# Kernel tuning notes

Hardware: AMD Instinct MI355X
Metric: run time of the kernel (lower is better)

## Reference

```python
import jax, jax.numpy as jnp
import numpy as np

NS, B, D_MODEL = 512, 2, 512
NH, DH = 8, 64
LEAKY_SLOPE = 0.01  # torch nn.LeakyReLU default


def setup_inputs() -> dict:
    key = jax.random.key(0)
    ks = jax.random.split(key, 6)
    scale = 1.0 / np.sqrt(D_MODEL)
    query = jax.random.normal(ks[0], (NS, B, D_MODEL), dtype=jnp.float32)
    W_q = jax.random.normal(ks[1], (D_MODEL, NH * DH), dtype=jnp.float32) * scale
    b_q = jnp.zeros((NH * DH,), dtype=jnp.float32)
    W_k = jax.random.normal(ks[2], (D_MODEL, NH * DH), dtype=jnp.float32) * scale
    b_k = jnp.zeros((NH * DH,), dtype=jnp.float32)
    # xavier_uniform over [NH, DH]
    bound = np.sqrt(6.0 / (NH + DH))
    scoring_proj = jax.random.uniform(ks[3], (NH, DH), minval=-bound, maxval=bound, dtype=jnp.float32)
    return {"query": query, "W_q": W_q, "b_q": b_q, "W_k": W_k, "b_k": b_k,
            "scoring_proj": scoring_proj}


def reference(query, W_q, b_q, W_k, b_k, scoring_proj):
    # query: [ns, b, d_model]
    q = query @ W_q + b_q  # [ns, b, nh*dh]
    k = query @ W_k + b_k  # [ns, b, nh*dh]
    # 'ns b (nh dh) -> b ns nh dh'
    q = jnp.transpose(q.reshape(NS, B, NH, DH), (1, 0, 2, 3))  # [b, ns, nh, dh]
    k = jnp.transpose(k.reshape(NS, B, NH, DH), (1, 0, 2, 3))  # [b, ns, nh, dh]
    # broadcast add: [b, q, k, nh, dh]
    s = q[:, :, None, :, :] + k[:, None, :, :, :]
    s = jnp.where(s >= 0, s, LEAKY_SLOPE * s)  # LeakyReLU
    attn = jnp.einsum('bqkhe,he->bhqk', s, scoring_proj)
    # k rearranged '(b nh) ns dh'
    k_out = jnp.transpose(k, (0, 2, 1, 3)).reshape(B * NH, NS, DH)
    return attn, k_out
```

## Files before the change

kernel.cpp:

```cpp
#include <hip/hip_runtime.h>

#define NS 512
#define DM 512
#define NH 8
#define DH 64
#define NHDH 512
#define ATTN_SIZE (2 * NH * NS * NS)

typedef __attribute__((ext_vector_type(8))) _Float16 half8;
typedef __attribute__((ext_vector_type(4))) float f32x4;
typedef _Float16 h2 __attribute__((ext_vector_type(2)));
typedef unsigned short ushort_t;
typedef __attribute__((ext_vector_type(2))) unsigned uint2v;

#if defined(__has_builtin)
#if __has_builtin(__builtin_amdgcn_fdot2)
#define HAVE_FDOT2 1
#endif
#if __has_builtin(__builtin_amdgcn_cvt_pkrtz)
#define HAVE_PKRTZ 1
#endif
#endif

__device__ __forceinline__ unsigned pkh(float a, float b) {
#ifdef HAVE_PKRTZ
    auto r = __builtin_amdgcn_cvt_pkrtz(a, b);
    return __builtin_bit_cast(unsigned, r);
#else
    h2 r; r[0] = (_Float16)a; r[1] = (_Float16)b;
    return __builtin_bit_cast(unsigned, r);
#endif
}

__device__ __forceinline__ float qdot2(unsigned w2, unsigned x2, float acc) {
#ifdef HAVE_FDOT2
    return __builtin_amdgcn_fdot2(__builtin_bit_cast(h2, w2),
                                  __builtin_bit_cast(h2, x2), acc, false);
#else
    h2 a = __builtin_bit_cast(h2, w2);
    h2 b = __builtin_bit_cast(h2, x2);
    return acc + (float)a[0] * (float)b[0] + (float)a[1] * (float)b[1];
#endif
}

__device__ __forceinline__ float dotabs(unsigned w2, unsigned q2, unsigned k2, float acc) {
    h2 s = __builtin_bit_cast(h2, q2) + __builtin_bit_cast(h2, k2);
    unsigned a = __builtin_bit_cast(unsigned, s) & 0x7FFF7FFFu;
    return qdot2(w2, a, acc);
}

__global__ __launch_bounds__(256) void proj_fused(
    const float* __restrict__ query,
    const float* __restrict__ Wq, const float* __restrict__ bq,
    const float* __restrict__ Wk, const float* __restrict__ bk,
    ushort_t* __restrict__ qh, ushort_t* __restrict__ kh,
    float* __restrict__ kout)
{
    const int h  = blockIdx.x;
    const int by = blockIdx.y;
    const int bz = blockIdx.z;
    const float* __restrict__ W   = bz ? Wk : Wq;
    const float* __restrict__ bia = bz ? bk : bq;
    ushort_t* __restrict__ hout = bz ? kh : qh;

    __shared__ __align__(16) ushort_t As[64][136];
    __shared__ __align__(16) ushort_t Bs[64][136];

    const int tid  = threadIdx.x;
    const int lane = tid & 63;
    const int wv   = __builtin_amdgcn_readfirstlane(tid >> 6);
    const int wr   = wv >> 1, wc = wv & 1;
    const int l15  = lane & 15, l4 = lane >> 4;

    float4 af[4][2];
    float  bf[8][4];
    #pragma unroll
    for (int i = 0; i < 4; ++i) {
        int s = i * 256 + tid;
        const float* src = query + (size_t)(by * 64 + (s >> 4)) * DM + (s & 15) * 8;
        af[i][0] = *(const float4*)(src);
        af[i][1] = *(const float4*)(src + 4);
    }
    #pragma unroll
    for (int p = 0; p < 8; ++p)
        #pragma unroll
        for (int j = 0; j < 4; ++j)
            bf[p][j] = W[(size_t)(p * 16 + (tid >> 6) * 4 + j) * NHDH + h * 64 + lane];

    f32x4 acc[2][2];
    #pragma unroll
    for (int f = 0; f < 2; ++f)
        #pragma unroll
        for (int g = 0; g < 2; ++g) acc[f][g] = (f32x4){0.f, 0.f, 0.f, 0.f};

    for (int kc = 0; kc < 4; ++kc) {
        __syncthreads();
        #pragma unroll
        for (int i = 0; i < 4; ++i) {
            int s = i * 256 + tid;
            uint4 pk;
            pk.x = pkh(af[i][0].x, af[i][0].y);
            pk.y = pkh(af[i][0].z, af[i][0].w);
            pk.z = pkh(af[i][1].x, af[i][1].y);
            pk.w = pkh(af[i][1].z, af[i][1].w);
            *(uint4*)&As[s >> 4][(s & 15) * 8] = pk;
        }
        #pragma unroll
        for (int p = 0; p < 8; ++p) {
            uint2v pk;
            pk.x = pkh(bf[p][0], bf[p][1]);
            pk.y = pkh(bf[p][2], bf[p][3]);
            *(uint2v*)&Bs[lane][p * 16 + (tid >> 6) * 4] = pk;
        }
        __syncthreads();
        if (kc < 3) {
            #pragma unroll
            for (int i = 0; i < 4; ++i) {
                int s = i * 256 + tid;
                const float* src = query + (size_t)(by * 64 + (s >> 4)) * DM
                                 + (kc + 1) * 128 + (s & 15) * 8;
                af[i][0] = *(const float4*)(src);
                af[i][1] = *(const float4*)(src + 4);
            }
            #pragma unroll
            for (int p = 0; p < 8; ++p)
                #pragma unroll
                for (int j = 0; j < 4; ++j)
                    bf[p][j] = W[(size_t)((kc + 1) * 128 + p * 16 + (tid >> 6) * 4 + j) * NHDH
                                 + h * 64 + lane];
        }
        #pragma unroll
        for (int ks = 0; ks < 4; ++ks) {
            half8 a0 = *(const half8*)&As[wr * 32 + l15     ][ks * 32 + l4 * 8];
            half8 a1 = *(const half8*)&As[wr * 32 + 16 + l15][ks * 32 + l4 * 8];
            half8 b0 = *(const half8*)&Bs[wc * 32 + l15     ][ks * 32 + l4 * 8];
            half8 b1 = *(const half8*)&Bs[wc * 32 + 16 + l15][ks * 32 + l4 * 8];
            acc[0][0] = __builtin_amdgcn_mfma_f32_16x16x32_f16(a0, b0, acc[0][0], 0, 0, 0);
            acc[0][1] = __builtin_amdgcn_mfma_f32_16x16x32_f16(a0, b1, acc[0][1], 0, 0, 0);
            acc[1][0] = __builtin_amdgcn_mfma_f32_16x16x32_f16(a1, b0, acc[1][0], 0, 0, 0);
            acc[1][1] = __builtin_amdgcn_mfma_f32_16x16x32_f16(a1, b1, acc[1][1], 0, 0, 0);
        }
    }

    const float bias0 = bia[h * 64 + wc * 32 + l15];
    const float bias1 = bia[h * 64 + wc * 32 + 16 + l15];
    #pragma unroll
    for (int f = 0; f < 2; ++f)
        #pragma unroll
        for (int g = 0; g < 2; ++g) {
            float bg = g ? bias1 : bias0;
            #pragma unroll
            for (int j = 0; j < 4; ++j) {
                int rt = wr * 32 + f * 16 + l4 * 4 + j;
                int ct = wc * 32 + g * 16 + l15;
                int rg = by * 64 + rt;
                int ns_ = rg >> 1, b_ = rg & 1;
                size_t idx = ((size_t)(b_ * NH + h) * NS + ns_) * DH + ct;
                float vv = acc[f][g][j] + bg;
                if (bz) kout[idx] = vv;
                _Float16 hv = (_Float16)vv;
                hout[idx] = __builtin_bit_cast(ushort_t, hv);
            }
        }
}

__global__ __launch_bounds__(256, 4) void attn3_kernel(
    const ushort_t* __restrict__ qh,
    const ushort_t* __restrict__ kh,
    const float* __restrict__ w,
    float* __restrict__ attn)
{
    __shared__ __align__(16) ushort_t Qs[32][72];

    const int tid  = threadIdx.x;
    const int lane = tid & 63;
    const int wv   = tid >> 6;
    const int bid  = blockIdx.x;
    const int kb   = bid & 3;
    const int bh   = (bid >> 2) & 15;
    const int qt   = bid >> 6;
    const int h    = bh & 7;

    const int c0 = kb * 128 + lane;
    const ushort_t* kb0 = kh + (size_t)bh * NS * DH + (size_t)c0 * DH;
    __align__(16) unsigned kr0[32], kr1[32];
    #pragma unroll
    for (int i = 0; i < 8; ++i)
        *(uint4*)&kr0[i * 4] = *(const uint4*)(kb0 + i * 8);
    #pragma unroll
    for (int i = 0; i < 8; ++i)
        *(uint4*)&kr1[i * 4] = *(const uint4*)(kb0 + 64 * DH + i * 8);

    {
        const uint4* qsrc = (const uint4*)(qh + (size_t)bh * NS * DH + (size_t)qt * 32 * DH);
        int row = tid >> 3, col = (tid & 7) * 8;
        *(uint4*)&Qs[row][col] = qsrc[tid];
    }

    unsigned wp[32];
    const float* wrow = w + h * DH;
    #pragma unroll
    for (int i = 0; i < 16; ++i) {
        float4 v = *(const float4*)(wrow + i * 4);
        _Float16 a = (_Float16)v.x, b = (_Float16)v.y, c = (_Float16)v.z, d = (_Float16)v.w;
        unsigned lo = (unsigned)__builtin_bit_cast(ushort_t, a) |
                      ((unsigned)__builtin_bit_cast(ushort_t, b) << 16);
        unsigned hi = (unsigned)__builtin_bit_cast(ushort_t, c) |
                      ((unsigned)__builtin_bit_cast(ushort_t, d) << 16);
        wp[2 * i]     = __builtin_amdgcn_readfirstlane(lo);
        wp[2 * i + 1] = __builtin_amdgcn_readfirstlane(hi);
    }

    float kd0 = 0.f, kd1 = 0.f;
    #pragma unroll
    for (int p = 0; p < 32; ++p) {
        kd0 = qdot2(wp[p], kr0[p], kd0);
        kd1 = qdot2(wp[p], kr1[p], kd1);
    }

    __syncthreads();

    float* obase = attn + (size_t)bh * NS * NS
                 + (size_t)(qt * 32 + wv * 8) * NS + kb * 128 + lane;

    #pragma unroll 2
    for (int r = 0; r < 8; ++r) {
        const int row = wv * 8 + r;
        __align__(16) unsigned q2a[32];
        #pragma unroll
        for (int i = 0; i < 8; ++i)
            *(uint4*)&q2a[i * 4] = *((const uint4*)&Qs[row][0] + i);

        float qd0 = 0.f, qd1 = 0.f;
        #pragma unroll
        for (int p = 0; p < 16; ++p) {
            qd0 = qdot2(wp[2 * p],     q2a[2 * p],     qd0);
            qd1 = qdot2(wp[2 * p + 1], q2a[2 * p + 1], qd1);
        }
        const float qd = qd0 + qd1;

        float a0 = 0.f, a1 = 0.f;
        #pragma unroll
        for (int p = 0; p < 32; ++p) {
            const unsigned q2 = q2a[p], w2 = wp[p];
            a0 = dotabs(w2, q2, kr0[p], a0);
            a1 = dotabs(w2, q2, kr1[p], a1);
        }

        float* ob = obase + r * NS;
        ob[0]  = fmaf(0.495f, a0, 0.505f * (qd + kd0));
        ob[64] = fmaf(0.495f, a1, 0.505f * (qd + kd1));
    }
}

extern "C" void kernel_launch(void* const* d_in, const int* in_sizes, int n_in,
                              void* d_out, int out_size, void* d_ws, size_t ws_size,
                              hipStream_t stream) {
    const float* query = (const float*)d_in[0];
    const float* Wq    = (const float*)d_in[1];
    const float* bq    = (const float*)d_in[2];
    const float* Wk    = (const float*)d_in[3];
    const float* bk    = (const float*)d_in[4];
    const float* w     = (const float*)d_in[5];

    float* attn = (float*)d_out;
    float* kout = (float*)d_out + ATTN_SIZE;

    char* ws = (char*)d_ws;
    ushort_t* qh = (ushort_t*)(ws);
    ushort_t* kh = (ushort_t*)(ws + (1u << 20));

    proj_fused<<<dim3(NH, 16, 2), 256, 0, stream>>>(query, Wq, bq, Wk, bk, qh, kh, kout);
    attn3_kernel<<<1024, 256, 0, stream>>>(qh, kh, w, attn);
}
```

Measured before the change: 33.61 us.

## Fuse projection and attention into one cooperative kernel with grid sync

Merges the projection and attention kernels into a single cooperative launch of 512 blocks that uses a grid-wide barrier between the two phases. Work is rebalanced so both phases use 512 blocks: projection tiles drop to 32 rows and attention blocks cover 64 query rows each. This is meant to remove the second kernel launch and the gap between kernels. In exchange it adds a grid barrier, per-call host queries for device attributes and occupancy, and lower per-block parallelism, with a two-kernel fallback if the cooperative launch is unavailable.

```diff
diff --git a/kernel.cpp b/kernel.cpp
--- a/kernel.cpp
+++ b/kernel.cpp
@@ -1,4 +1,7 @@
 #include <hip/hip_runtime.h>
+#include <hip/hip_cooperative_groups.h>
+
+namespace cg = cooperative_groups;
 
 #define NS 512
 #define DM 512
@@ -6,6 +9,7 @@
 #define DH 64
 #define NHDH 512
 #define ATTN_SIZE (2 * NH * NS * NS)
+#define SMEM_BYTES 26112
 
 typedef __attribute__((ext_vector_type(8))) _Float16 half8;
 typedef __attribute__((ext_vector_type(4))) float f32x4;
@@ -49,35 +53,34 @@
     return qdot2(w2, a, acc);
 }
 
-__global__ __launch_bounds__(256) void proj_fused(
+__device__ __forceinline__ void phase_proj(int bid, int tid,
     const float* __restrict__ query,
     const float* __restrict__ Wq, const float* __restrict__ bq,
     const float* __restrict__ Wk, const float* __restrict__ bk,
     ushort_t* __restrict__ qh, ushort_t* __restrict__ kh,
-    float* __restrict__ kout)
-{
-    const int h  = blockIdx.x;
-    const int by = blockIdx.y;
-    const int bz = blockIdx.z;
+    float* __restrict__ kout, char* smem)
+{
+    const int h   = bid & 7;
+    const int byt = (bid >> 3) & 31;
+    const int bz  = bid >> 8;
     const float* __restrict__ W   = bz ? Wk : Wq;
     const float* __restrict__ bia = bz ? bk : bq;
     ushort_t* __restrict__ hout = bz ? kh : qh;
 
-    __shared__ __align__(16) ushort_t As[64][136];
-    __shared__ __align__(16) ushort_t Bs[64][136];
-
-    const int tid  = threadIdx.x;
+    ushort_t (*As)[136] = (ushort_t(*)[136])smem;
+    ushort_t (*Bs)[136] = (ushort_t(*)[136])(smem + 32 * 136 * 2);
+
     const int lane = tid & 63;
-    const int wv   = __builtin_amdgcn_readfirstlane(tid >> 6);
-    const int wr   = wv >> 1, wc = wv & 1;
+    const int w4   = tid >> 6;
+    const int wr   = w4 >> 1, wc = w4 & 1;
     const int l15  = lane & 15, l4 = lane >> 4;
 
-    float4 af[4][2];
+    float4 af[2][2];
     float  bf[8][4];
     #pragma unroll
-    for (int i = 0; i < 4; ++i) {
+    for (int i = 0; i < 2; ++i) {
         int s = i * 256 + tid;
-        const float* src = query + (size_t)(by * 64 + (s >> 4)) * DM + (s & 15) * 8;
+        const float* src = query + (size_t)(byt * 32 + (s >> 4)) * DM + (s & 15) * 8;
         af[i][0] = *(const float4*)(src);
         af[i][1] = *(const float4*)(src + 4);
     }
@@ -85,18 +88,16 @@
     for (int p = 0; p < 8; ++p)
         #pragma unroll
         for (int j = 0; j < 4; ++j)
-            bf[p][j] = W[(size_t)(p * 16 + (tid >> 6) * 4 + j) * NHDH + h * 64 + lane];
-
-    f32x4 acc[2][2];
-    #pragma unroll
-    for (int f = 0; f < 2; ++f)
-        #pragma unroll
-        for (int g = 0; g < 2; ++g) acc[f][g] = (f32x4){0.f, 0.f, 0.f, 0.f};
+            bf[p][j] = W[(size_t)(p * 16 + w4 * 4 + j) * NHDH + h * 64 + lane];
+
+    f32x4 acc[2];
+    acc[0] = (f32x4){0.f, 0.f, 0.f, 0.f};
+    acc[1] = (f32x4){0.f, 0.f, 0.f, 0.f};
 
     for (int kc = 0; kc < 4; ++kc) {
         __syncthreads();
         #pragma unroll
-        for (int i = 0; i < 4; ++i) {
+        for (int i = 0; i < 2; ++i) {
             int s = i * 256 + tid;
             uint4 pk;
             pk.x = pkh(af[i][0].x, af[i][0].y);
@@ -110,14 +111,14 @@
             uint2v pk;
             pk.x = pkh(bf[p][0], bf[p][1]);
             pk.y = pkh(bf[p][2], bf[p][3]);
-            *(uint2v*)&Bs[lane][p * 16 + (tid >> 6) * 4] = pk;
+            *(uint2v*)&Bs[lane][p * 16 + w4 * 4] = pk;
         }
         __syncthreads();
         if (kc < 3) {
             #pragma unroll
-            for (int i = 0; i < 4; ++i) {
+            for (int i = 0; i < 2; ++i) {
                 int s = i * 256 + tid;
-                const float* src = query + (size_t)(by * 64 + (s >> 4)) * DM
+                const float* src = query + (size_t)(byt * 32 + (s >> 4)) * DM
                                  + (kc + 1) * 128 + (s & 15) * 8;
                 af[i][0] = *(const float4*)(src);
                 af[i][1] = *(const float4*)(src + 4);
@@ -126,59 +127,48 @@
             for (int p = 0; p < 8; ++p)
                 #pragma unroll
                 for (int j = 0; j < 4; ++j)
-                    bf[p][j] = W[(size_t)((kc + 1) * 128 + p * 16 + (tid >> 6) * 4 + j) * NHDH
+                    bf[p][j] = W[(size_t)((kc + 1) * 128 + p * 16 + w4 * 4 + j) * NHDH
                                  + h * 64 + lane];
         }
         #pragma unroll
         for (int ks = 0; ks < 4; ++ks) {
-            half8 a0 = *(const half8*)&As[wr * 32 + l15     ][ks * 32 + l4 * 8];
-            half8 a1 = *(const half8*)&As[wr * 32 + 16 + l15][ks * 32 + l4 * 8];
+            half8 a0 = *(const half8*)&As[wr * 16 + l15     ][ks * 32 + l4 * 8];
             half8 b0 = *(const half8*)&Bs[wc * 32 + l15     ][ks * 32 + l4 * 8];
             half8 b1 = *(const half8*)&Bs[wc * 32 + 16 + l15][ks * 32 + l4 * 8];
-            acc[0][0] = __builtin_amdgcn_mfma_f32_16x16x32_f16(a0, b0, acc[0][0], 0, 0, 0);
-            acc[0][1] = __builtin_amdgcn_mfma_f32_16x16x32_f16(a0, b1, acc[0][1], 0, 0, 0);
-            acc[1][0] = __builtin_amdgcn_mfma_f32_16x16x32_f16(a1, b0, acc[1][0], 0, 0, 0);
-            acc[1][1] = __builtin_amdgcn_mfma_f32_16x16x32_f16(a1, b1, acc[1][1], 0, 0, 0);
-        }
-    }
-
-    const float bias0 = bia[h * 64 + wc * 32 + l15];
-    const float bias1 = bia[h * 64 + wc * 32 + 16 + l15];
-    #pragma unroll
-    for (int f = 0; f < 2; ++f)
-        #pragma unroll
-        for (int g = 0; g < 2; ++g) {
-            float bg = g ? bias1 : bias0;
-            #pragma unroll
-            for (int j = 0; j < 4; ++j) {
-                int rt = wr * 32 + f * 16 + l4 * 4 + j;
-                int ct = wc * 32 + g * 16 + l15;
-                int rg = by * 64 + rt;
-                int ns_ = rg >> 1, b_ = rg & 1;
-                size_t idx = ((size_t)(b_ * NH + h) * NS + ns_) * DH + ct;
-                float vv = acc[f][g][j] + bg;
-                if (bz) kout[idx] = vv;
-                _Float16 hv = (_Float16)vv;
-                hout[idx] = __builtin_bit_cast(ushort_t, hv);
-            }
-        }
-}
-
-__global__ __launch_bounds__(256, 4) void attn3_kernel(
-    const ushort_t* __restrict__ qh,
-    const ushort_t* __restrict__ kh,
-    const float* __restrict__ w,
-    float* __restrict__ attn)
-{
-    __shared__ __align__(16) ushort_t Qs[32][72];
-
-    const int tid  = threadIdx.x;
+            acc[0] = __builtin_amdgcn_mfma_f32_16x16x32_f16(a0, b0, acc[0], 0, 0, 0);
+            acc[1] = __builtin_amdgcn_mfma_f32_16x16x32_f16(a0, b1, acc[1], 0, 0, 0);
+        }
+    }
+
+    #pragma unroll
+    for (int g = 0; g < 2; ++g) {
+        const float bg = bia[h * 64 + wc * 32 + g * 16 + l15];
+        #pragma unroll
+        for (int j = 0; j < 4; ++j) {
+            int rt = wr * 16 + l4 * 4 + j;
+            int ct = wc * 32 + g * 16 + l15;
+            int rg = byt * 32 + rt;
+            int ns_ = rg >> 1, b_ = rg & 1;
+            size_t idx = ((size_t)(b_ * NH + h) * NS + ns_) * DH + ct;
+            float vv = acc[g][j] + bg;
+            if (bz) kout[idx] = vv;
+            _Float16 hv = (_Float16)vv;
+            hout[idx] = __builtin_bit_cast(ushort_t, hv);
+        }
+    }
+}
+
+__device__ __forceinline__ void phase_attn(int bid, int tid,
+    const ushort_t* __restrict__ qh, const ushort_t* __restrict__ kh,
+    const float* __restrict__ w, float* __restrict__ attn, char* smem)
+{
+    ushort_t (*Qs)[72] = (ushort_t(*)[72])smem;
+
     const int lane = tid & 63;
     const int wv   = tid >> 6;
-    const int bid  = blockIdx.x;
     const int kb   = bid & 3;
     const int bh   = (bid >> 2) & 15;
-    const int qt   = bid >> 6;
+    const int qg   = bid >> 6;
     const int h    = bh & 7;
 
     const int c0 = kb * 128 + lane;
@@ -192,9 +182,12 @@
         *(uint4*)&kr1[i * 4] = *(const uint4*)(kb0 + 64 * DH + i * 8);
 
     {
-        const uint4* qsrc = (const uint4*)(qh + (size_t)bh * NS * DH + (size_t)qt * 32 * DH);
-        int row = tid >> 3, col = (tid & 7) * 8;
-        *(uint4*)&Qs[row][col] = qsrc[tid];
+        const uint4* qsrc = (const uint4*)(qh + (size_t)bh * NS * DH + (size_t)qg * 64 * DH);
+        #pragma unroll
+        for (int i = 0; i < 2; ++i) {
+            int s = i * 256 + tid;
+            *(uint4*)&Qs[s >> 3][(s & 7) * 8] = qsrc[s];
+        }
     }
 
     unsigned wp[32];
@@ -220,37 +213,74 @@
 
     __syncthreads();
 
-    float* obase = attn + (size_t)bh * NS * NS
-                 + (size_t)(qt * 32 + wv * 8) * NS + kb * 128 + lane;
-
-    #pragma unroll 2
-    for (int r = 0; r < 8; ++r) {
-        const int row = wv * 8 + r;
-        __align__(16) unsigned q2a[32];
-        #pragma unroll
-        for (int i = 0; i < 8; ++i)
-            *(uint4*)&q2a[i * 4] = *((const uint4*)&Qs[row][0] + i);
-
-        float qd0 = 0.f, qd1 = 0.f;
-        #pragma unroll
-        for (int p = 0; p < 16; ++p) {
-            qd0 = qdot2(wp[2 * p],     q2a[2 * p],     qd0);
-            qd1 = qdot2(wp[2 * p + 1], q2a[2 * p + 1], qd1);
-        }
-        const float qd = qd0 + qd1;
-
-        float a0 = 0.f, a1 = 0.f;
-        #pragma unroll
-        for (int p = 0; p < 32; ++p) {
-            const unsigned q2 = q2a[p], w2 = wp[p];
-            a0 = dotabs(w2, q2, kr0[p], a0);
-            a1 = dotabs(w2, q2, kr1[p], a1);
-        }
-
-        float* ob = obase + r * NS;
-        ob[0]  = fmaf(0.495f, a0, 0.505f * (qd + kd0));
-        ob[64] = fmaf(0.495f, a1, 0.505f * (qd + kd1));
-    }
+    #pragma unroll
+    for (int t = 0; t < 2; ++t) {
+        float* obase = attn + (size_t)bh * NS * NS
+                     + (size_t)(qg * 64 + t * 32 + wv * 8) * NS + kb * 128 + lane;
+        #pragma unroll 2
+        for (int r = 0; r < 8; ++r) {
+            const int row = t * 32 + wv * 8 + r;
+            __align__(16) unsigned q2a[32];
+            #pragma unroll
+            for (int i = 0; i < 8; ++i)
+                *(uint4*)&q2a[i * 4] = *((const uint4*)&Qs[row][0] + i);
+
+            float qd0 = 0.f, qd1 = 0.f;
+            #pragma unroll
+            for (int p = 0; p < 16; ++p) {
+                qd0 = qdot2(wp[2 * p],     q2a[2 * p],     qd0);
+                qd1 = qdot2(wp[2 * p + 1], q2a[2 * p + 1], qd1);
+            }
+            const float qd = qd0 + qd1;
+
+            float a0 = 0.f, a1 = 0.f;
+            #pragma unroll
+            for (int p = 0; p < 32; ++p) {
+                const unsigned q2 = q2a[p], w2 = wp[p];
+                a0 = dotabs(w2, q2, kr0[p], a0);
+                a1 = dotabs(w2, q2, kr1[p], a1);
+            }
+
+            float* ob = obase + r * NS;
+            ob[0]  = fmaf(0.495f, a0, 0.505f * (qd + kd0));
+            ob[64] = fmaf(0.495f, a1, 0.505f * (qd + kd1));
+        }
+    }
+}
+
+__global__ __launch_bounds__(256, 4) void fused2(
+    const float* __restrict__ query,
+    const float* __restrict__ Wq, const float* __restrict__ bq,
+    const float* __restrict__ Wk, const float* __restrict__ bk,
+    const float* __restrict__ w,
+    ushort_t* __restrict__ qh, ushort_t* __restrict__ kh,
+    float* __restrict__ kout, float* __restrict__ attn)
+{
+    cg::grid_group grid = cg::this_grid();
+    __shared__ __align__(16) char smem[SMEM_BYTES];
+    const int bid = blockIdx.x, tid = threadIdx.x;
+
+    phase_proj(bid, tid, query, Wq, bq, Wk, bk, qh, kh, kout, smem);
+    grid.sync();
+    phase_attn(bid, tid, qh, kh, w, attn, smem);
+}
+
+__global__ __launch_bounds__(256, 4) void kProj(
+    const float* __restrict__ query,
+    const float* __restrict__ Wq, const float* __restrict__ bq,
+    const float* __restrict__ Wk, const float* __restrict__ bk,
+    ushort_t* __restrict__ qh, ushort_t* __restrict__ kh, float* __restrict__ kout)
+{
+    __shared__ __align__(16) char smem[SMEM_BYTES];
+    phase_proj(blockIdx.x, threadIdx.x, query, Wq, bq, Wk, bk, qh, kh, kout, smem);
+}
+
+__global__ __launch_bounds__(256, 4) void kAttn(
+    const ushort_t* __restrict__ qh, const ushort_t* __restrict__ kh,
+    const float* __restrict__ w, float* __restrict__ attn)
+{
+    __shared__ __align__(16) char smem[SMEM_BYTES];
+    phase_attn(blockIdx.x, threadIdx.x, qh, kh, w, attn, smem);
 }
 
 extern "C" void kernel_launch(void* const* d_in, const int* in_sizes, int n_in,
@@ -270,6 +300,23 @@
     ushort_t* qh = (ushort_t*)(ws);
     ushort_t* kh = (ushort_t*)(ws + (1u << 20));
 
-    proj_fused<<<dim3(NH, 16, 2), 256, 0, stream>>>(query, Wq, bq, Wk, bk, qh, kh, kout);
-    attn3_kernel<<<1024, 256, 0, stream>>>(qh, kh, w, attn);
-}
+    int dev = 0;
+    (void)hipGetDevice(&dev);
+    int nCU = 0, coopAttr = 0, maxB = 0;
+    (void)hipDeviceGetAttribute(&nCU, hipDeviceAttributeMultiprocessorCount, dev);
+    (void)hipDeviceGetAttribute(&coopAttr, hipDeviceAttributeCooperativeLaunch, dev);
+    hipError_t oe = hipOccupancyMaxActiveBlocksPerMultiprocessor(
+        &maxB, (const void*)fused2, 256, 0);
+
+    if (coopAttr && oe == hipSuccess && (long)maxB * nCU >= 512) {
+        void* args[] = {(void*)&query, (void*)&Wq, (void*)&bq, (void*)&Wk, (void*)&bk,
+                        (void*)&w, (void*)&qh, (void*)&kh, (void*)&kout, (void*)&attn};
+        hipError_t le = hipLaunchCooperativeKernel((const void*)fused2,
+                                                   dim3(512), dim3(256),
+                                                   args, 0, stream);
+        if (le == hipSuccess) return;
+    }
+
+    kProj<<<512, 256, 0, stream>>>(query, Wq, bq, Wk, bk, qh, kh, kout);
+    kAttn<<<512, 256, 0, stream>>>(qh, kh, w, attn);
+}
```

Measured after the change: 96.35 us. 187% more time.

## Fuse Q/K projection into the attention-score kernel, recomputing projections per tile

Applied to the files above, without the earlier changes.

Merges the projection GEMM and the additive-attention scoring into one kernel. Each block computes its own 64 query rows and 128 key rows of projections with MFMA into registers, then stages them in shared memory, so there is no fp16 workspace round-trip and one fewer launch. This costs redundant projection work, since K tiles are recomputed by every query tile and Q tiles by every key tile. It also halves the block count to 512 and doubles the rows each block handles.

```diff
diff --git a/kernel.cpp b/kernel.cpp
--- a/kernel.cpp
+++ b/kernel.cpp
@@ -49,166 +49,131 @@
     return qdot2(w2, a, acc);
 }
 
-__global__ __launch_bounds__(256) void proj_fused(
-    const float* __restrict__ query,
-    const float* __restrict__ Wq, const float* __restrict__ bq,
-    const float* __restrict__ Wk, const float* __restrict__ bk,
-    ushort_t* __restrict__ qh, ushort_t* __restrict__ kh,
-    float* __restrict__ kout)
+__global__ __attribute__((amdgpu_flat_work_group_size(256, 256),
+                          amdgpu_waves_per_eu(2, 4)))
+void fused6(const float* __restrict__ query,
+            const float* __restrict__ Wq, const float* __restrict__ bq,
+            const float* __restrict__ Wk, const float* __restrict__ bk,
+            const float* __restrict__ w,
+            float* __restrict__ kout, float* __restrict__ attn)
 {
-    const int h  = blockIdx.x;
-    const int by = blockIdx.y;
-    const int bz = blockIdx.z;
-    const float* __restrict__ W   = bz ? Wk : Wq;
-    const float* __restrict__ bia = bz ? bk : bq;
-    ushort_t* __restrict__ hout = bz ? kh : qh;
-
-    __shared__ __align__(16) ushort_t As[64][136];
-    __shared__ __align__(16) ushort_t Bs[64][136];
+    __shared__ __align__(16) char smem[34816];
+    ushort_t (*As)[136] = (ushort_t(*)[136])smem;
+    ushort_t (*Bs)[136] = (ushort_t(*)[136])(smem + 17408);
+    ushort_t (*Qt)[72]  = (ushort_t(*)[72])smem;
+    ushort_t (*Kt)[72]  = (ushort_t(*)[72])(smem + 9216);
 
     const int tid  = threadIdx.x;
-    const int lane = tid & 63;
-    const int wv   = __builtin_amdgcn_readfirstlane(tid >> 6);
-    const int wr   = wv >> 1, wc = wv & 1;
-    const int l15  = lane & 15, l4 = lane >> 4;
-
-    float4 af[4][2];
-    float  bf[8][4];
-    #pragma unroll
-    for (int i = 0; i < 4; ++i) {
-        int s = i * 256 + tid;
-        const float* src = query + (size_t)(by * 64 + (s >> 4)) * DM + (s & 15) * 8;
-        af[i][0] = *(const float4*)(src);
-        af[i][1] = *(const float4*)(src + 4);
-    }
-    #pragma unroll
-    for (int p = 0; p < 8; ++p)
-        #pragma unroll
-        for (int j = 0; j < 4; ++j)
-            bf[p][j] = W[(size_t)(p * 16 + (tid >> 6) * 4 + j) * NHDH + h * 64 + lane];
-
-    f32x4 acc[2][2];
-    #pragma unroll
-    for (int f = 0; f < 2; ++f)
-        #pragma unroll
-        for (int g = 0; g < 2; ++g) acc[f][g] = (f32x4){0.f, 0.f, 0.f, 0.f};
-
-    for (int kc = 0; kc < 4; ++kc) {
-        __syncthreads();
-        #pragma unroll
-        for (int i = 0; i < 4; ++i) {
-            int s = i * 256 + tid;
-            uint4 pk;
-            pk.x = pkh(af[i][0].x, af[i][0].y);
-            pk.y = pkh(af[i][0].z, af[i][0].w);
-            pk.z = pkh(af[i][1].x, af[i][1].y);
-            pk.w = pkh(af[i][1].z, af[i][1].w);
-            *(uint4*)&As[s >> 4][(s & 15) * 8] = pk;
-        }
-        #pragma unroll
-        for (int p = 0; p < 8; ++p) {
-            uint2v pk;
-            pk.x = pkh(bf[p][0], bf[p][1]);
-            pk.y = pkh(bf[p][2], bf[p][3]);
-            *(uint2v*)&Bs[lane][p * 16 + (tid >> 6) * 4] = pk;
-        }
-        __syncthreads();
-        if (kc < 3) {
-            #pragma unroll
-            for (int i = 0; i < 4; ++i) {
-                int s = i * 256 + tid;
-                const float* src = query + (size_t)(by * 64 + (s >> 4)) * DM
-                                 + (kc + 1) * 128 + (s & 15) * 8;
-                af[i][0] = *(const float4*)(src);
-                af[i][1] = *(const float4*)(src + 4);
-            }
-            #pragma unroll
-            for (int p = 0; p < 8; ++p)
-                #pragma unroll
-                for (int j = 0; j < 4; ++j)
-                    bf[p][j] = W[(size_t)((kc + 1) * 128 + p * 16 + (tid >> 6) * 4 + j) * NHDH
-                                 + h * 64 + lane];
-        }
-        #pragma unroll
-        for (int ks = 0; ks < 4; ++ks) {
-            half8 a0 = *(const half8*)&As[wr * 32 + l15     ][ks * 32 + l4 * 8];
-            half8 a1 = *(const half8*)&As[wr * 32 + 16 + l15][ks * 32 + l4 * 8];
-            half8 b0 = *(const half8*)&Bs[wc * 32 + l15     ][ks * 32 + l4 * 8];
-            half8 b1 = *(const half8*)&Bs[wc * 32 + 16 + l15][ks * 32 + l4 * 8];
-            acc[0][0] = __builtin_amdgcn_mfma_f32_16x16x32_f16(a0, b0, acc[0][0], 0, 0, 0);
-            acc[0][1] = __builtin_amdgcn_mfma_f32_16x16x32_f16(a0, b1, acc[0][1], 0, 0, 0);
-            acc[1][0] = __builtin_amdgcn_mfma_f32_16x16x32_f16(a1, b0, acc[1][0], 0, 0, 0);
-            acc[1][1] = __builtin_amdgcn_mfma_f32_16x16x32_f16(a1, b1, acc[1][1], 0, 0, 0);
-        }
-    }
-
-    const float bias0 = bia[h * 64 + wc * 32 + l15];
-    const float bias1 = bia[h * 64 + wc * 32 + 16 + l15];
-    #pragma unroll
-    for (int f = 0; f < 2; ++f)
-        #pragma unroll
-        for (int g = 0; g < 2; ++g) {
-            float bg = g ? bias1 : bias0;
-            #pragma unroll
-            for (int j = 0; j < 4; ++j) {
-                int rt = wr * 32 + f * 16 + l4 * 4 + j;
-                int ct = wc * 32 + g * 16 + l15;
-                int rg = by * 64 + rt;
-                int ns_ = rg >> 1, b_ = rg & 1;
-                size_t idx = ((size_t)(b_ * NH + h) * NS + ns_) * DH + ct;
-                float vv = acc[f][g][j] + bg;
-                if (bz) kout[idx] = vv;
-                _Float16 hv = (_Float16)vv;
-                hout[idx] = __builtin_bit_cast(ushort_t, hv);
-            }
-        }
-}
-
-__global__ __launch_bounds__(256, 4) void attn3_kernel(
-    const ushort_t* __restrict__ qh,
-    const ushort_t* __restrict__ kh,
-    const float* __restrict__ w,
-    float* __restrict__ attn)
-{
-    __shared__ __align__(16) ushort_t Qs[32][72];
-
-    const int tid  = threadIdx.x;
-    const int lane = tid & 63;
-    const int wv   = tid >> 6;
     const int bid  = blockIdx.x;
-    const int kb   = bid & 3;
+    const int kt   = bid & 3;
     const int bh   = (bid >> 2) & 15;
     const int qt   = bid >> 6;
+    const int b    = bh >> 3;
     const int h    = bh & 7;
 
-    const int c0 = kb * 128 + lane;
-    const ushort_t* kb0 = kh + (size_t)bh * NS * DH + (size_t)c0 * DH;
+    const int lane = tid & 63;
+    const int w4   = tid >> 6;
+    const int l15  = lane & 15, l4 = lane >> 4;
+
+    f32x4 acc[3][4];
+    #pragma unroll
+    for (int g = 0; g < 3; ++g)
+        #pragma unroll
+        for (int cf = 0; cf < 4; ++cf) acc[g][cf] = (f32x4){0.f, 0.f, 0.f, 0.f};
+
+    const int nsb[3] = {qt * 64, kt * 128, kt * 128 + 64};
+
+    for (int kc = 0; kc < 4; ++kc) {
+        #pragma unroll
+        for (int g = 0; g < 3; ++g) {
+            __syncthreads();
+            if (g < 2) {
+                const float* __restrict__ W = g ? Wk : Wq;
+                float bf[8][4];
+                #pragma unroll
+                for (int p = 0; p < 8; ++p)
+                    #pragma unroll
+                    for (int j = 0; j < 4; ++j)
+                        bf[p][j] = W[(size_t)(kc * 128 + p * 16 + w4 * 4 + j) * NHDH
+                                     + h * 64 + lane];
+                #pragma unroll
+                for (int p = 0; p < 8; ++p) {
+                    uint2v pk;
+                    pk.x = pkh(bf[p][0], bf[p][1]);
+                    pk.y = pkh(bf[p][2], bf[p][3]);
+                    *(uint2v*)&Bs[lane][p * 16 + w4 * 4] = pk;
+                }
+            }
+            {
+                const int base = nsb[g];
+                #pragma unroll
+                for (int i = 0; i < 4; ++i) {
+                    int s = i * 256 + tid;
+                    int r = s >> 4, q8 = s & 15;
+                    const float* src = query + (size_t)(2 * (base + r) + b) * DM
+                                     + kc * 128 + q8 * 8;
+                    float4 v0 = *(const float4*)(src);
+                    float4 v1 = *(const float4*)(src + 4);
+                    uint4 pk;
+                    pk.x = pkh(v0.x, v0.y);
+                    pk.y = pkh(v0.z, v0.w);
+                    pk.z = pkh(v1.x, v1.y);
+                    pk.w = pkh(v1.z, v1.w);
+                    *(uint4*)&As[r][q8 * 8] = pk;
+                }
+            }
+            __syncthreads();
+            #pragma unroll
+            for (int cf = 0; cf < 4; ++cf)
+                #pragma unroll
+                for (int ks = 0; ks < 4; ++ks) {
+                    half8 a = *(const half8*)&As[w4 * 16 + l15][ks * 32 + l4 * 8];
+                    half8 bb = *(const half8*)&Bs[cf * 16 + l15][ks * 32 + l4 * 8];
+                    acc[g][cf] = __builtin_amdgcn_mfma_f32_16x16x32_f16(a, bb, acc[g][cf], 0, 0, 0);
+                }
+        }
+    }
+
+    __syncthreads();
+    #pragma unroll
+    for (int g = 0; g < 3; ++g) {
+        const float* __restrict__ bia = g ? bk : bq;
+        #pragma unroll
+        for (int cf = 0; cf < 4; ++cf) {
+            const int col = cf * 16 + l15;
+            const float bg = bia[h * 64 + col];
+            #pragma unroll
+            for (int j = 0; j < 4; ++j) {
+                const int row = w4 * 16 + l4 * 4 + j;
+                float v = acc[g][cf][j] + bg;
+                _Float16 hv = (_Float16)v;
+                if (g == 0) {
+                    Qt[row][col] = __builtin_bit_cast(ushort_t, hv);
+                } else {
+                    Kt[(g - 1) * 64 + row][col] = __builtin_bit_cast(ushort_t, hv);
+                    if (qt == 0)
+                        kout[((size_t)(b * NH + h) * NS + kt * 128 + (g - 1) * 64 + row) * DH + col] = v;
+                }
+            }
+        }
+    }
+    __syncthreads();
+
     __align__(16) unsigned kr0[32], kr1[32];
     #pragma unroll
     for (int i = 0; i < 8; ++i)
-        *(uint4*)&kr0[i * 4] = *(const uint4*)(kb0 + i * 8);
+        *(uint4*)&kr0[i * 4] = *(const uint4*)&Kt[lane][i * 8];
     #pragma unroll
     for (int i = 0; i < 8; ++i)
-        *(uint4*)&kr1[i * 4] = *(const uint4*)(kb0 + 64 * DH + i * 8);
-
-    {
-        const uint4* qsrc = (const uint4*)(qh + (size_t)bh * NS * DH + (size_t)qt * 32 * DH);
-        int row = tid >> 3, col = (tid & 7) * 8;
-        *(uint4*)&Qs[row][col] = qsrc[tid];
-    }
+        *(uint4*)&kr1[i * 4] = *(const uint4*)&Kt[64 + lane][i * 8];
 
     unsigned wp[32];
     const float* wrow = w + h * DH;
     #pragma unroll
     for (int i = 0; i < 16; ++i) {
         float4 v = *(const float4*)(wrow + i * 4);
-        _Float16 a = (_Float16)v.x, b = (_Float16)v.y, c = (_Float16)v.z, d = (_Float16)v.w;
-        unsigned lo = (unsigned)__builtin_bit_cast(ushort_t, a) |
-                      ((unsigned)__builtin_bit_cast(ushort_t, b) << 16);
-        unsigned hi = (unsigned)__builtin_bit_cast(ushort_t, c) |
-                      ((unsigned)__builtin_bit_cast(ushort_t, d) << 16);
-        wp[2 * i]     = __builtin_amdgcn_readfirstlane(lo);
-        wp[2 * i + 1] = __builtin_amdgcn_readfirstlane(hi);
+        wp[2 * i]     = (unsigned)__builtin_amdgcn_readfirstlane((int)pkh(v.x, v.y));
+        wp[2 * i + 1] = (unsigned)__builtin_amdgcn_readfirstlane((int)pkh(v.z, v.w));
     }
 
     float kd0 = 0.f, kd1 = 0.f;
@@ -218,38 +183,38 @@
         kd1 = qdot2(wp[p], kr1[p], kd1);
     }
 
-    __syncthreads();
-
-    float* obase = attn + (size_t)bh * NS * NS
-                 + (size_t)(qt * 32 + wv * 8) * NS + kb * 128 + lane;
-
-    #pragma unroll 2
-    for (int r = 0; r < 8; ++r) {
-        const int row = wv * 8 + r;
-        __align__(16) unsigned q2a[32];
-        #pragma unroll
-        for (int i = 0; i < 8; ++i)
-            *(uint4*)&q2a[i * 4] = *((const uint4*)&Qs[row][0] + i);
-
-        float qd0 = 0.f, qd1 = 0.f;
-        #pragma unroll
-        for (int p = 0; p < 16; ++p) {
-            qd0 = qdot2(wp[2 * p],     q2a[2 * p],     qd0);
-            qd1 = qdot2(wp[2 * p + 1], q2a[2 * p + 1], qd1);
+    #pragma unroll
+    for (int t = 0; t < 2; ++t) {
+        float* obase = attn + (size_t)bh * NS * NS
+                     + (size_t)(qt * 64 + t * 32 + w4 * 8) * NS + kt * 128 + lane;
+        #pragma unroll 2
+        for (int r = 0; r < 8; ++r) {
+            const int row = t * 32 + w4 * 8 + r;
+            __align__(16) unsigned q2a[32];
+            #pragma unroll
+            for (int i = 0; i < 8; ++i)
+                *(uint4*)&q2a[i * 4] = *(const uint4*)&Qt[row][i * 8];
+
+            float qd0 = 0.f, qd1 = 0.f;
+            #pragma unroll
+            for (int p = 0; p < 16; ++p) {
+                qd0 = qdot2(wp[2 * p],     q2a[2 * p],     qd0);
+                qd1 = qdot2(wp[2 * p + 1], q2a[2 * p + 1], qd1);
+            }
+            const float qd = qd0 + qd1;
+
+            float a0 = 0.f, a1 = 0.f;
+            #pragma unroll
+            for (int p = 0; p < 32; ++p) {
+                const unsigned q2 = q2a[p], w2 = wp[p];
+                a0 = dotabs(w2, q2, kr0[p], a0);
+                a1 = dotabs(w2, q2, kr1[p], a1);
+            }
+
+            float* ob = obase + r * NS;
+            ob[0]  = fmaf(0.495f, a0, 0.505f * (qd + kd0));
+            ob[64] = fmaf(0.495f, a1, 0.505f * (qd + kd1));
         }
-        const float qd = qd0 + qd1;
-
-        float a0 = 0.f, a1 = 0.f;
-        #pragma unroll
-        for (int p = 0; p < 32; ++p) {
-            const unsigned q2 = q2a[p], w2 = wp[p];
-            a0 = dotabs(w2, q2, kr0[p], a0);
-            a1 = dotabs(w2, q2, kr1[p], a1);
-        }
-
-        float* ob = obase + r * NS;
-        ob[0]  = fmaf(0.495f, a0, 0.505f * (qd + kd0));
-        ob[64] = fmaf(0.495f, a1, 0.505f * (qd + kd1));
     }
 }
 
@@ -266,10 +231,6 @@
     float* attn = (float*)d_out;
     float* kout = (float*)d_out + ATTN_SIZE;
 
-    char* ws = (char*)d_ws;
-    ushort_t* qh = (ushort_t*)(ws);
-    ushort_t* kh = (ushort_t*)(ws + (1u << 20));
-
-    proj_fused<<<dim3(NH, 16, 2), 256, 0, stream>>>(query, Wq, bq, Wk, bk, qh, kh, kout);
-    attn3_kernel<<<1024, 256, 0, stream>>>(qh, kh, w, attn);
-}
+    fused6<<<dim3(512), dim3(256), 0, stream>>>(query, Wq, bq, Wk, bk, w,
+                                                kout, attn);
+}
```

New measurement: 47.45 us. 41.2% more time.
